# Optimization experiments

Hardware: AMD Instinct MI355X
Metric: run time of the kernel (lower is better)

Reference implementation:

```python
import jax, jax.numpy as jnp
import numpy as np

FEATURE_DIM = 256  # matches __init__(feature_dim); sqrt_dim = sqrt(256)
RECORD_LEN = np.array([4, 3, 4, 4, 3, 4, 2, 4], dtype=np.int64)  # cav counts per sample, sum = 28


def setup_inputs() -> dict:
    key = jax.random.key(0)
    N = int(RECORD_LEN.sum())
    x = jax.random.normal(key, (N, 256, 128, 128), dtype=jnp.float32)  # [N, C, W, H]
    return {"x": x, "record_len": RECORD_LEN}


def reference(x, record_len):
    # record_len is a host-side (numpy) int array: group sizes are static shapes.
    lens = [int(l) for l in np.asarray(record_len)]
    C, W, H = x.shape[1], x.shape[2], x.shape[3]
    d = W * H
    inv_sqrt_dim = np.float32(1.0 / np.sqrt(FEATURE_DIM))
    outs = []
    start = 0
    for L in lens:
        # raw view of [L, C, W*H] into [C, L, W*H], matching torch .view semantics
        xx = x[start:start + L].reshape(C, L, d)
        score = jnp.einsum('cqd,ckd->cqk', xx, xx) * inv_sqrt_dim  # [C, L, L]
        attn = jax.nn.softmax(score, axis=-1)
        ctx = jnp.einsum('cqk,ckd->cqd', attn, xx)  # [C, L, d]
        h = ctx.reshape(L, C, W, H)[0]  # ego vehicle's fused feature
        outs.append(h)
        start += L
    return jnp.stack(outs)  # [num_groups, C, W, H]
```

## Files before the change

### kernel.cpp

```cpp
#include <hip/hip_runtime.h>
#include <math.h>


#define DIMD 16384
#define NCH  256
#define ROW4 4096

typedef float f32x4 __attribute__((ext_vector_type(4)));

template <int L>
__device__ __forceinline__ void do_cluster(const float* __restrict__ base,
                                           float* __restrict__ outp,
                                           int nout, int tid) {
    constexpr int NP  = L * (L + 1) / 2;
    constexpr int PER = ROW4 / 1024;
    __shared__ float red[16][NP];
    __shared__ float S_l[NP];

    const int lane = tid & 63, wave = tid >> 6;

    float4 v[L][PER];
    #pragma unroll
    for (int k = 0; k < L; ++k) {
        const float4* row = (const float4*)(base + (size_t)k * DIMD);
        #pragma unroll
        for (int i = 0; i < PER; ++i) v[k][i] = row[i * 1024 + tid];
    }

    float acc[NP];
    #pragma unroll
    for (int p = 0; p < NP; ++p) acc[p] = 0.f;
    #pragma unroll
    for (int i = 0; i < PER; ++i) {
        int idx = 0;
        #pragma unroll
        for (int a = 0; a < L; ++a) {
            #pragma unroll
            for (int b = a; b < L; ++b) {
                acc[idx] = fmaf(v[a][i].x, v[b][i].x, acc[idx]);
                acc[idx] = fmaf(v[a][i].y, v[b][i].y, acc[idx]);
                acc[idx] = fmaf(v[a][i].z, v[b][i].z, acc[idx]);
                acc[idx] = fmaf(v[a][i].w, v[b][i].w, acc[idx]);
                ++idx;
            }
        }
    }

    #pragma unroll
    for (int p = 0; p < NP; ++p) {
        float s = acc[p];
        #pragma unroll
        for (int off = 32; off > 0; off >>= 1) s += __shfl_down(s, off, 64);
        if (lane == 0) red[wave][p] = s;
    }
    __syncthreads();
    if (tid < NP) {
        float s = 0.f;
        #pragma unroll
        for (int w = 0; w < 16; ++w) s += red[w][tid];
        S_l[tid] = s * 0.0625f;
    }
    __syncthreads();

    float S[L][L];
    {
        int idx = 0;
        #pragma unroll
        for (int a = 0; a < L; ++a)
            #pragma unroll
            for (int b = a; b < L; ++b) { const float s = S_l[idx]; S[a][b] = s; S[b][a] = s; ++idx; }
    }
    float W[L][L];
    #pragma unroll
    for (int q = 0; q < L; ++q) {
        float m = S[q][0];
        #pragma unroll
        for (int k = 1; k < L; ++k) m = fmaxf(m, S[q][k]);
        float den = 0.f;
        #pragma unroll
        for (int k = 0; k < L; ++k) { W[q][k] = expf(S[q][k] - m); den += W[q][k]; }
        const float inv = 1.0f / den;
        #pragma unroll
        for (int k = 0; k < L; ++k) W[q][k] *= inv;
    }

    for (int q = 0; q < nout; ++q) {
        float* orow = outp + (size_t)q * DIMD;
        #pragma unroll
        for (int i = 0; i < PER; ++i) {
            float4 o = {0.f, 0.f, 0.f, 0.f};
            #pragma unroll
            for (int k = 0; k < L; ++k) {
                const float w = W[q][k];
                o.x = fmaf(w, v[k][i].x, o.x);
                o.y = fmaf(w, v[k][i].y, o.y);
                o.z = fmaf(w, v[k][i].z, o.z);
                o.w = fmaf(w, v[k][i].w, o.w);
            }
            f32x4 ov = {o.x, o.y, o.z, o.w};
            __builtin_nontemporal_store(ov, (f32x4*)((float4*)orow + i * 1024 + tid));
        }
    }
}

__global__ __launch_bounds__(1024, 4) void attfusion_regresident(const float* __restrict__ x,
                                                                 float* __restrict__ out) {
    const int starts[8] = {0, 4, 7, 11, 15, 18, 22, 24};
    const int g4[5] = {0, 2, 3, 5, 7};
    const int g3[2] = {1, 4};

    const int b = blockIdx.x;
    int g, c, L;
    if (b < 320)      { g = g4[b >> 6];        c = b & 63;          L = 4; }
    else if (b < 492) { g = g3[(b - 320) / 86]; c = (b - 320) % 86; L = 3; }
    else              { g = 6;                  c = b - 492;        L = 2; }

    const float* base = x + ((size_t)starts[g] * NCH + (size_t)c * L) * DIMD;
    float* outp = out + ((size_t)g * NCH + (size_t)c * L) * DIMD;
    const int nout = min(L, NCH - c * L);
    const int tid = threadIdx.x;

    if (L == 4)      do_cluster<4>(base, outp, nout, tid);
    else if (L == 3) do_cluster<3>(base, outp, nout, tid);
    else             do_cluster<2>(base, outp, nout, tid);
}

extern "C" void kernel_launch(void* const* d_in, const int* in_sizes, int n_in,
                              void* d_out, int out_size, void* d_ws, size_t ws_size,
                              hipStream_t stream) {
    const float* x = (const float*)d_in[0];
    float* out = (float*)d_out;
    attfusion_regresident<<<dim3(620), dim3(1024), 0, stream>>>(x, out);
}
```

Measured before the change: 49.88 us.

## Chain multiple clusters per block with a 257-block balanced grid

Replaces the one-cluster-per-block grid of 620 blocks with 257 blocks. Each block loops over up to four cluster slots, assigned so every block moves a similar amount of data. The shared-memory reduction buffers are hoisted to the kernel and sized for the largest cluster so every slot can reuse them. The aim is to remove the partial tail wave of blocks and balance work across the CUs. The cost is fewer resident waves per CU, so less memory latency is hidden, and each slot's load, compute and store phases run back to back.

```diff
diff --git a/kernel.cpp b/kernel.cpp
--- a/kernel.cpp
+++ b/kernel.cpp
@@ -11,11 +11,11 @@
 template <int L>
 __device__ __forceinline__ void do_cluster(const float* __restrict__ base,
                                            float* __restrict__ outp,
-                                           int nout, int tid) {
+                                           int nout, int tid,
+                                           float (*__restrict__ red)[10],
+                                           float* __restrict__ S_l) {
     constexpr int NP  = L * (L + 1) / 2;
     constexpr int PER = ROW4 / 1024;
-    __shared__ float red[16][NP];
-    __shared__ float S_l[NP];
 
     const int lane = tid & 63, wave = tid >> 6;
 
@@ -103,26 +103,54 @@
     }
 }
 
-__global__ __launch_bounds__(1024, 4) void attfusion_regresident(const float* __restrict__ x,
-                                                                 float* __restrict__ out) {
+__device__ __forceinline__ bool chain_slot(int b, int s, int& g, int& c, int& L) {
+    const int g4[5] = {0, 2, 3, 5, 7};
+    if (b < 160) {
+        if (s >= 2) return false;
+        const int i = b * 2 + s;
+        g = g4[i >> 6]; c = i & 63; L = 4;
+        return true;
+    }
+    if (b < 246) {
+        const int j = b - 160;
+        if (s < 2) {
+            const int i = j * 2 + s;
+            g = (i < 86) ? 1 : 4; c = (i < 86) ? i : i - 86; L = 3;
+            return true;
+        }
+        if (s == 2) { g = 6; c = j; L = 2; return true; }
+        return false;
+    }
+    if (b < 256) {
+        const int j = b - 246;
+        if (s >= 4) return false;
+        g = 6; c = 86 + j * 4 + s; L = 2;
+        return true;
+    }
+    if (s >= 2) return false;
+    g = 6; c = 126 + s; L = 2;
+    return true;
+}
+
+__global__ __launch_bounds__(1024, 4) void attfusion_chain(const float* __restrict__ x,
+                                                           float* __restrict__ out) {
+    __shared__ float red[16][10];
+    __shared__ float S_l[10];
     const int starts[8] = {0, 4, 7, 11, 15, 18, 22, 24};
-    const int g4[5] = {0, 2, 3, 5, 7};
-    const int g3[2] = {1, 4};
-
     const int b = blockIdx.x;
-    int g, c, L;
-    if (b < 320)      { g = g4[b >> 6];        c = b & 63;          L = 4; }
-    else if (b < 492) { g = g3[(b - 320) / 86]; c = (b - 320) % 86; L = 3; }
-    else              { g = 6;                  c = b - 492;        L = 2; }
-
-    const float* base = x + ((size_t)starts[g] * NCH + (size_t)c * L) * DIMD;
-    float* outp = out + ((size_t)g * NCH + (size_t)c * L) * DIMD;
-    const int nout = min(L, NCH - c * L);
     const int tid = threadIdx.x;
 
-    if (L == 4)      do_cluster<4>(base, outp, nout, tid);
-    else if (L == 3) do_cluster<3>(base, outp, nout, tid);
-    else             do_cluster<2>(base, outp, nout, tid);
+    #pragma unroll 1
+    for (int s = 0; s < 4; ++s) {
+        int g, c, L;
+        if (!chain_slot(b, s, g, c, L)) break;
+        const float* base = x + ((size_t)starts[g] * NCH + (size_t)c * L) * DIMD;
+        float* outp = out + ((size_t)g * NCH + (size_t)c * L) * DIMD;
+        const int nout = min(L, NCH - c * L);
+        if (L == 4)      do_cluster<4>(base, outp, nout, tid, red, S_l);
+        else if (L == 3) do_cluster<3>(base, outp, nout, tid, red, S_l);
+        else             do_cluster<2>(base, outp, nout, tid, red, S_l);
+    }
 }
 
 extern "C" void kernel_launch(void* const* d_in, const int* in_sizes, int n_in,
@@ -130,5 +158,5 @@
                               hipStream_t stream) {
     const float* x = (const float*)d_in[0];
     float* out = (float*)d_out;
-    attfusion_regresident<<<dim3(620), dim3(1024), 0, stream>>>(x, out);
+    attfusion_chain<<<dim3(257), dim3(1024), 0, stream>>>(x, out);
 }
```

Result: faster. 47.45 us (-4.9%).
